# Optimization experiments

Measured on AMD Instinct MI355X. Metric: run time of the kernel, lower is better.

## Reference

```python
import jax, jax.numpy as jnp
import numpy as np
from jax import lax

B, A, SEQ, FIN = 512, 16, 50, 6
H, H2, T, G, S = 256, 128, 60, 64, 6
GR0, GR1 = -50.0, 50.0
CELL = (GR1 - GR0) / G
NTYPES, EMB = 10, 16
NENC, NL = 5, 2

def setup_inputs() -> dict:
    key = jax.random.key(0)
    ks = jax.random.split(key, 40)
    def rn(k, shape, scale=0.05):
        return (jax.random.normal(k, shape) * scale).astype(jnp.float32)
    history = jax.random.normal(ks[0], (B, A, SEQ, FIN), dtype=jnp.float32)
    types = jax.random.randint(ks[1], (B,), 0, NTYPES)
    history = history.at[:, 0, 0, 5].set(types.astype(jnp.float32))
    d = dict(history=history)
    d['emb'] = rn(ks[2], (NTYPES, EMB))
    d['fe_W1'] = rn(ks[3], (FIN + EMB, H)); d['fe_b1'] = jnp.zeros((H,), jnp.float32)
    d['fe_W2'] = rn(ks[4], (H, H));        d['fe_b2'] = jnp.zeros((H,), jnp.float32)
    d['enc_Wih'] = rn(ks[5], (NENC, NL, H, 3 * H))
    d['enc_Whh'] = rn(ks[6], (NENC, NL, H, 3 * H))
    d['enc_bih'] = rn(ks[7], (NENC, NL, 3 * H))
    d['enc_bhh'] = rn(ks[8], (NENC, NL, 3 * H))
    d['dec_Wih0'] = rn(ks[9], (2, 3 * H)); d['dec_Whh0'] = rn(ks[10], (H, 3 * H))
    d['dec_bih0'] = rn(ks[11], (3 * H));   d['dec_bhh0'] = rn(ks[12], (3 * H))
    d['dec_Wih1'] = rn(ks[13], (H, 3 * H)); d['dec_Whh1'] = rn(ks[14], (H, 3 * H))
    d['dec_bih1'] = rn(ks[15], (3 * H));    d['dec_bhh1'] = rn(ks[16], (3 * H))
    d['hg_W1'] = rn(ks[17], (H, H));   d['hg_b1'] = jnp.zeros((H,), jnp.float32)
    d['hg_W2'] = rn(ks[18], (H, H2));  d['hg_b2'] = jnp.zeros((H2,), jnp.float32)
    d['hg_W3'] = rn(ks[19], (H2, T * 2)); d['hg_b3'] = jnp.zeros((T * 2,), jnp.float32)
    d['ce_W1'] = rn(ks[20], (H, H2));  d['ce_b1'] = jnp.zeros((H2,), jnp.float32)
    d['ce_W2'] = rn(ks[21], (H2, T));  d['ce_b2'] = jnp.zeros((T,), jnp.float32)
    d['hp_W1'] = rn(ks[22], (H, H));   d['hp_b1'] = jnp.zeros((H,), jnp.float32)
    d['hp_W2'] = rn(ks[23], (H, G * G)); d['hp_b2'] = jnp.zeros((G * G,), jnp.float32)
    return d

def _gru_cell(xt, h, Wih, Whh, bih, bhh):
    # torch GRU gate order: r, z, n
    gi = xt @ Wih + bih
    gh = h @ Whh + bhh
    Hd = h.shape[-1]
    r = jax.nn.sigmoid(gi[:, :Hd] + gh[:, :Hd])
    z = jax.nn.sigmoid(gi[:, Hd:2 * Hd] + gh[:, Hd:2 * Hd])
    n = jnp.tanh(gi[:, 2 * Hd:] + r * gh[:, 2 * Hd:])
    return (1.0 - z) * n + z * h

def _forward(history, emb, fe_W1, fe_b1, fe_W2, fe_b2,
             enc_Wih, enc_Whh, enc_bih, enc_bhh,
             dec_Wih0, dec_Whh0, dec_bih0, dec_bhh0,
             dec_Wih1, dec_Whh1, dec_bih1, dec_bhh1,
             hg_W1, hg_b1, hg_W2, hg_b2, hg_W3, hg_b3,
             ce_W1, ce_b1, ce_W2, ce_b2, hp_W1, hp_b1, hp_W2, hp_b2):
    ego = history[:, 0]                                   # [B,SEQ,6]
    etype = jnp.clip(ego[:, 0, 5].astype(jnp.int32), 0, 9)
    # type -> encoder index (vehicle,pedestrian,cyclist,bus,default)
    eidx = jnp.array([0, 1, 4, 2, 3, 4, 4, 4, 4, 4], jnp.int32)[etype]
    te = emb[etype]                                       # [B,16]
    x_in = jnp.concatenate([ego, jnp.broadcast_to(te[:, None, :], (B, SEQ, EMB))], axis=-1)
    feat = jax.nn.relu(x_in @ fe_W1 + fe_b1) @ fe_W2 + fe_b2  # [B,SEQ,H]

    # 2-layer GRU with per-example (type-gathered) weights
    x_cur = feat.transpose(1, 0, 2)                       # [SEQ,B,H]
    h_finals = []
    for l in range(NL):
        Wih = enc_Wih[eidx, l]; Whh = enc_Whh[eidx, l]    # [B,H,3H]
        bih = enc_bih[eidx, l]; bhh = enc_bhh[eidx, l]    # [B,3H]
        def step(h, xt, Wih=Wih, Whh=Whh, bih=bih, bhh=bhh):
            gi = jnp.einsum('bd,bdg->bg', xt, Wih) + bih
            gh = jnp.einsum('bh,bhg->bg', h, Whh) + bhh
            r = jax.nn.sigmoid(gi[:, :H] + gh[:, :H])
            z = jax.nn.sigmoid(gi[:, H:2 * H] + gh[:, H:2 * H])
            n = jnp.tanh(gi[:, 2 * H:] + r * gh[:, 2 * H:])
            hn = (1.0 - z) * n + z * h
            return hn, hn
        h_last, ys = lax.scan(step, jnp.zeros((B, H), feat.dtype), x_cur)
        x_cur = ys
        h_finals.append(h_last)
    enc_h0, enc_h1 = h_finals

    # decoder GRU, single timestep: x = last ego position
    x0 = ego[:, -1, :2]
    h0 = _gru_cell(x0, enc_h0, dec_Wih0, dec_Whh0, dec_bih0, dec_bhh0)
    h1 = _gru_cell(h0, enc_h1, dec_Wih1, dec_Whh1, dec_bih1, dec_bhh1)
    last_hidden = h1                                      # [B,H]

    traj = (jax.nn.relu(jax.nn.relu(last_hidden @ hg_W1 + hg_b1) @ hg_W2 + hg_b2) @ hg_W3 + hg_b3)
    traj = traj.reshape(B, T, 2)
    conf = jax.nn.relu(last_hidden @ ce_W1 + ce_b1) @ ce_W2 + ce_b2   # [B,T]

    key = jax.random.key(42)
    k_noise, k_samp = jax.random.split(key)
    noise = jax.random.normal(k_noise, (T, B, H), last_hidden.dtype)
    scale = (0.1 * jnp.arange(T, dtype=last_hidden.dtype) / T)[:, None, None]
    th = last_hidden[None] + noise * scale                # [T,B,H]
    logits = jax.nn.relu(th @ hp_W1 + hp_b1) @ hp_W2 + hp_b2  # [T,B,G*G]

    # vectorized multinomial over (samples, timesteps, batch)
    idx = jax.random.categorical(k_samp, logits, shape=(S - 1, T, B))  # int [S-1,T,B]
    x_idx = (idx % G).astype(jnp.float32)
    y_idx = (idx // G).astype(jnp.float32)
    pts = jnp.stack([GR0 + x_idx * CELL + CELL / 2,
                     GR0 + y_idx * CELL + CELL / 2], axis=-1)  # [S-1,T,B,2]
    pts = pts.transpose(2, 0, 1, 3)                       # [B,S-1,T,2]

    predictions = jnp.concatenate([traj[:, None], pts], axis=1)  # [B,S,T,2]
    decay = jnp.float32(0.9) ** jnp.arange(S, dtype=jnp.float32)
    confidences = conf.mean(axis=1)[:, None] * decay[None, :]    # [B,S]
    return predictions, confidences

def reference(history, emb, fe_W1, fe_b1, fe_W2, fe_b2,
              enc_Wih, enc_Whh, enc_bih, enc_bhh,
              dec_Wih0, dec_Whh0, dec_bih0, dec_bhh0,
              dec_Wih1, dec_Whh1, dec_bih1, dec_bhh1,
              hg_W1, hg_b1, hg_W2, hg_b2, hg_W3, hg_b3,
              ce_W1, ce_b1, ce_W2, ce_b2, hp_W1, hp_b1, hp_W2, hp_b2):
    return _forward(history, emb, fe_W1, fe_b1, fe_W2, fe_b2,
                    enc_Wih, enc_Whh, enc_bih, enc_bhh,
                    dec_Wih0, dec_Whh0, dec_bih0, dec_bhh0,
                    dec_Wih1, dec_Whh1, dec_bih1, dec_bhh1,
                    hg_W1, hg_b1, hg_W2, hg_b2, hg_W3, hg_b3,
                    ce_W1, ce_b1, ce_W2, ce_b2, hp_W1, hp_b1, hp_W2, hp_b2)
```

## Files before the change

### kernel.cpp

```cpp
#include <hip/hip_runtime.h>
#include <stdint.h>
#include <math.h>

#define JAX_PARTITIONABLE 1

#define B_ 512
#define SEQ_ 50
#define H_ 256
#define H2_ 128
#define T_ 60
#define S_ 6
#define EMB_ 16
#define NL_ 2
#define TG_ 768
#define CAT_ 4096
#define GUMBEL_N 629145600u
#define NOISE_N 7864320u

typedef float f32x2 __attribute__((ext_vector_type(2)));

#define PKFMA_LO(acc, w, h) \
  asm("v_pk_fma_f32 %0, %1, %2, %0 op_sel:[0,0,0] op_sel_hi:[1,0,1]" : "+v"(acc) : "v"(w), "v"(h))
#define PKFMA_HI(acc, w, h) \
  asm("v_pk_fma_f32 %0, %1, %2, %0 op_sel:[0,1,0] op_sel_hi:[1,1,1]" : "+v"(acc) : "v"(w), "v"(h))

__host__ __device__ inline uint32_t rotl32(uint32_t x, int r) {
#if defined(__HIP_DEVICE_COMPILE__)
  return __builtin_amdgcn_alignbit(x, x, 32 - r);
#else
  return (x << r) | (x >> (32 - r));
#endif
}

__host__ __device__ inline void tf2x32(uint32_t k0, uint32_t k1, uint32_t x0, uint32_t x1,
                                       uint32_t& o0, uint32_t& o1) {
  uint32_t ks2 = k0 ^ k1 ^ 0x1BD11BDAu;
  x0 += k0; x1 += k1;
#define TFR(r) do { x0 += x1; x1 = rotl32(x1, r); x1 ^= x0; } while (0)
  TFR(13); TFR(15); TFR(26); TFR(6);
  x0 += k1; x1 += ks2 + 1u;
  TFR(17); TFR(29); TFR(16); TFR(24);
  x0 += ks2; x1 += k0 + 2u;
  TFR(13); TFR(15); TFR(26); TFR(6);
  x0 += k0; x1 += k1 + 3u;
  TFR(17); TFR(29); TFR(16); TFR(24);
  x0 += k1; x1 += ks2 + 4u;
  TFR(13); TFR(15); TFR(26); TFR(6);
  x0 += ks2; x1 += k0 + 5u;
#undef TFR
  o0 = x0; o1 = x1;
}

__device__ inline uint32_t jax_bits(uint32_t k0, uint32_t k1, uint32_t i, uint32_t n) {
#if JAX_PARTITIONABLE
  (void)n;
  uint32_t a, b;
  tf2x32(k0, k1, 0u, i, a, b);
  return a ^ b;
#else
  uint32_t half = n >> 1;
  uint32_t lo = (i < half) ? i : (i - half);
  uint32_t a, b;
  tf2x32(k0, k1, lo, lo + half, a, b);
  return (i < half) ? a : b;
#endif
}

__device__ inline float bits_to_f01(uint32_t bits) {
  return __uint_as_float((bits >> 9) | 0x3f800000u) - 1.0f;
}

__device__ inline float erfinv_f(float x) {
  double xd = (double)x;
  float w = (float)(-log((1.0 - xd) * (1.0 + xd)));
  float p;
  if (w < 5.0f) {
    w = __fadd_rn(w, -2.5f);
    p = 2.81022636e-08f;
    p = __fadd_rn(3.43273939e-07f, __fmul_rn(p, w));
    p = __fadd_rn(-3.5233877e-06f, __fmul_rn(p, w));
    p = __fadd_rn(-4.39150654e-06f, __fmul_rn(p, w));
    p = __fadd_rn(0.00021858087f, __fmul_rn(p, w));
    p = __fadd_rn(-0.00125372503f, __fmul_rn(p, w));
    p = __fadd_rn(-0.00417768164f, __fmul_rn(p, w));
    p = __fadd_rn(0.246640727f, __fmul_rn(p, w));
    p = __fadd_rn(1.50140941f, __fmul_rn(p, w));
  } else {
    w = __fadd_rn(__fsqrt_rn(w), -3.0f);
    p = -0.000200214257f;
    p = __fadd_rn(0.000100950558f, __fmul_rn(p, w));
    p = __fadd_rn(0.00134934322f, __fmul_rn(p, w));
    p = __fadd_rn(-0.00367342844f, __fmul_rn(p, w));
    p = __fadd_rn(0.00573950773f, __fmul_rn(p, w));
    p = __fadd_rn(-0.0076224613f, __fmul_rn(p, w));
    p = __fadd_rn(0.00943887047f, __fmul_rn(p, w));
    p = __fadd_rn(1.00167406f, __fmul_rn(p, w));
    p = __fadd_rn(2.83297682f, __fmul_rn(p, w));
  }
  return __fmul_rn(p, x);
}

__device__ inline float gumbel_f32(uint32_t bits) {
  float f = bits_to_f01(bits);
  float u = fmaxf(f, 1.17549435e-38f);
  float l1 = logf(u);
  return -logf(-l1);
}

__device__ inline uint32_t orderkey(float s) {
  uint32_t sb = __float_as_uint(s);
  return (sb & 0x80000000u) ? ~sb : (sb | 0x80000000u);
}

__global__ __launch_bounds__(512) void k_init(const float* __restrict__ hist,
                                              float* __restrict__ x0buf, int* __restrict__ ip) {
  int b = threadIdx.x;
  if (b < B_) {
    float tv = hist[b * 4800 + 5];
    int et = (int)tv;
    et = et < 0 ? 0 : (et > 9 ? 9 : et);
    const int mp[10] = {0, 1, 4, 2, 3, 4, 4, 4, 4, 4};
    ip[b] = et;
    ip[512 + b] = mp[et];
    x0buf[b * 2 + 0] = hist[b * 4800 + 49 * 6 + 0];
    x0buf[b * 2 + 1] = hist[b * 4800 + 49 * 6 + 1];
  }
  __syncthreads();
  if (b == 0) {
    int cnt[5] = {0, 0, 0, 0, 0};
    for (int i = 0; i < B_; i++) cnt[ip[512 + i]]++;
    int off[6];
    off[0] = 0;
    for (int e = 0; e < 5; e++) off[e + 1] = off[e] + cnt[e];
    int pos[5];
    for (int e = 0; e < 5; e++) pos[e] = off[e];
    for (int i = 0; i < B_; i++) { int e = ip[512 + i]; ip[1024 + pos[e]++] = i; }
    int* tbl = ip + 1536;
    int nrt = 0;
    for (int e = 0; e < 5; e++) {
      int n = cnt[e];
      for (int s = 0; s < n; s += 16) {
        tbl[1 + nrt] = e;
        tbl[37 + nrt] = off[e] + s;
        tbl[73 + nrt] = (n - s) < 16 ? (n - s) : 16;
        nrt++;
      }
    }
    tbl[0] = nrt;
  }
}

__global__ void k_zero(uint32_t* p, int n) {
  int i = blockIdx.x * blockDim.x + threadIdx.x;
  if (i < n) p[i] = 0u;
}

__global__ __launch_bounds__(256) void k_feat(const float* __restrict__ hist, const float* __restrict__ emb,
    const float* __restrict__ W1, const float* __restrict__ b1,
    const float* __restrict__ W2, const float* __restrict__ b2,
    const int* __restrict__ ip, float* __restrict__ featbuf) {
  __shared__ float xs[16][22];
  __shared__ float t1[16][H_];
  int row0 = blockIdx.x * 16;
  int tid = threadIdx.x;
  for (int idx = tid; idx < 16 * 22; idx += 256) {
    int r = idx / 22, c = idx % 22;
    int g = row0 + r;
    int b = g / SEQ_, s = g % SEQ_;
    xs[r][c] = (c < 6) ? hist[b * 4800 + s * 6 + c] : emb[ip[b] * EMB_ + (c - 6)];
  }
  __syncthreads();
  int j = tid;
  {
    double acc[16];
    for (int r = 0; r < 16; r++) acc[r] = 0.0;
    for (int k = 0; k < 22; k++) {
      double w = (double)W1[k * H_ + j];
      for (int r = 0; r < 16; r++) acc[r] += (double)xs[r][k] * w;
    }
    double bb = (double)b1[j];
    for (int r = 0; r < 16; r++) t1[r][j] = fmaxf((float)(acc[r] + bb), 0.0f);
  }
  __syncthreads();
  {
    double acc[16];
    for (int r = 0; r < 16; r++) acc[r] = 0.0;
    for (int k = 0; k < H_; k++) {
      double w = (double)W2[k * H_ + j];
      for (int r = 0; r < 16; r++) acc[r] += (double)t1[r][k] * w;
    }
    double bb = (double)b2[j];
    for (int r = 0; r < 16; r++) {
      float v = (float)(acc[r] + bb);
      int g = row0 + r;
      int b = g / SEQ_, s = g % SEQ_;
      featbuf[(size_t)s * (B_ * H_) + (size_t)b * H_ + j] = v;
    }
  }
}

__device__ __forceinline__ void gi_block(float (*xs)[H_], int* rowb,
    int rt, int cg, int tid,
    const float* __restrict__ x, float* __restrict__ gi_out,
    const float* __restrict__ Wih_base, const float* __restrict__ bih_base,
    int layer, const int* __restrict__ ip) {
  const int* tbl = ip + 1536;
  const int* order = ip + 1024;
  int nrt = tbl[0];
  if (rt >= nrt) return;
  int e = tbl[1 + rt];
  int start = tbl[37 + rt];
  int nr = tbl[73 + rt];
  for (int idx = tid; idx < 16 * H_; idx += 256) {
    int r = idx >> 8, k = idx & 255;
    int rr = (r < nr) ? r : 0;
    int b = order[start + rr];
    if (k == 0) rowb[r] = b;
    xs[r][k] = x[b * H_ + k];
  }
  __syncthreads();
  size_t woff = (size_t)(e * NL_ + layer);
  const float* Wih = Wih_base + woff * (size_t)H_ * TG_;
  const float* bih = bih_base + woff * TG_;
  int j = tid & 31, rs = tid >> 5;
  int c = cg * 32 + j;
  int cr = c, cz = H_ + c, cn = 2 * H_ + c;
  double ar0 = 0, ar1 = 0, az0 = 0, az1 = 0, an0 = 0, an1 = 0;
  for (int k = 0; k < H_; k++) {
    float wr = Wih[k * TG_ + cr], wz = Wih[k * TG_ + cz], wn = Wih[k * TG_ + cn];
    float x0 = xs[rs][k], x1 = xs[rs + 8][k];
    ar0 += (double)x0 * wr; ar1 += (double)x1 * wr;
    az0 += (double)x0 * wz; az1 += (double)x1 * wz;
    an0 += (double)x0 * wn; an1 += (double)x1 * wn;
  }
  double br = (double)bih[cr], bz = (double)bih[cz], bn = (double)bih[cn];
  for (int p = 0; p < 2; p++) {
    int r = rs + 8 * p;
    if (r >= nr) continue;
    int b = rowb[r];
    gi_out[b * TG_ + cr] = (float)((p ? ar1 : ar0) + br);
    gi_out[b * TG_ + cz] = (float)((p ? az1 : az0) + bz);
    gi_out[b * TG_ + cn] = (float)((p ? an1 : an0) + bn);
  }
}

__device__ __forceinline__ void step_block(float (*hs)[H_], int* rowb,
    int rt, int cg, int tid,
    const float* __restrict__ gi_in, const float* __restrict__ hin,
    float* __restrict__ hout, float* __restrict__ ys,
    const float* __restrict__ Whh_base, const float* __restrict__ bhh_base,
    int layer, const int* __restrict__ ip) {
  const int* tbl = ip + 1536;
  const int* order = ip + 1024;
  int nrt = tbl[0];
  if (rt >= nrt) return;
  int e = tbl[1 + rt];
  int start = tbl[37 + rt];
  int nr = tbl[73 + rt];
  for (int idx = tid; idx < 16 * H_; idx += 256) {
    int r = idx >> 8, k = idx & 255;
    int rr = (r < nr) ? r : 0;
    int b = order[start + rr];
    if (k == 0) rowb[r] = b;
    hs[r][k] = hin[b * H_ + k];
  }
  __syncthreads();
  size_t woff = (size_t)(e * NL_ + layer);
  const float* Whh = Whh_base + woff * (size_t)H_ * TG_;
  const float* bhh = bhh_base + woff * TG_;
  int j = tid & 31, rs = tid >> 5;
  int c = cg * 32 + j;
  int cr = c, cz = H_ + c, cn = 2 * H_ + c;
  double gr0 = 0, gr1 = 0, gz0 = 0, gz1 = 0, gn0 = 0, gn1 = 0;
  for (int k = 0; k < H_; k++) {
    float wr = Whh[k * TG_ + cr], wz = Whh[k * TG_ + cz], wn = Whh[k * TG_ + cn];
    float h0 = hs[rs][k], h1 = hs[rs + 8][k];
    gr0 += (double)h0 * wr; gr1 += (double)h1 * wr;
    gz0 += (double)h0 * wz; gz1 += (double)h1 * wz;
    gn0 += (double)h0 * wn; gn1 += (double)h1 * wn;
  }
  double bhr = (double)bhh[cr], bhz = (double)bhh[cz], bhn = (double)bhh[cn];
  for (int p = 0; p < 2; p++) {
    int r = rs + 8 * p;
    if (r >= nr) continue;
    int b = rowb[r];
    double gir = (double)gi_in[b * TG_ + cr];
    double giz = (double)gi_in[b * TG_ + cz];
    double gin = (double)gi_in[b * TG_ + cn];
    double ghr = (p ? gr1 : gr0) + bhr;
    double ghz = (p ? gz1 : gz0) + bhz;
    double ghn = (p ? gn1 : gn0) + bhn;
    double rr = 1.0 / (1.0 + exp(-(gir + ghr)));
    double zz = 1.0 / (1.0 + exp(-(giz + ghz)));
    double nn = tanh(gin + rr * ghn);
    double hv = (double)hs[r][c];
    float hnew = (float)((1.0 - zz) * nn + zz * hv);
    hout[b * H_ + c] = hnew;
    if (ys) ys[b * H_ + c] = hnew;
  }
}

__global__ __launch_bounds__(256) void k_pipe(int d,
    const float* __restrict__ feat, float* __restrict__ ys0,
    float* __restrict__ gi0, float* __restrict__ gi1,
    float* __restrict__ h0A, float* __restrict__ h0B,
    float* __restrict__ h1A, float* __restrict__ h1B,
    const float* __restrict__ Wih, const float* __restrict__ Whh,
    const float* __restrict__ bih, const float* __restrict__ bhh,
    const int* __restrict__ ip) {
  __shared__ float sb[16][H_];
  __shared__ int rowb[16];
  int g = blockIdx.x;
  int grp = g / 288, bx = g % 288;
  int rt = bx >> 3, cg = bx & 7;
  int tid = threadIdx.x;
  if (grp == 0) {
    int t = d; if (t >= SEQ_) return;
    gi_block(sb, rowb, rt, cg, tid, feat + (size_t)t * 131072,
             gi0 + (size_t)(t & 1) * 393216, Wih, bih, 0, ip);
  } else if (grp == 1) {
    int t = d - 1; if (t < 0 || t >= SEQ_) return;
    const float* hin = (t & 1) ? h0B : h0A;
    float* hout = (t & 1) ? h0A : h0B;
    step_block(sb, rowb, rt, cg, tid, gi0 + (size_t)(t & 1) * 393216,
               hin, hout, ys0 + (size_t)t * 131072, Whh, bhh, 0, ip);
  } else if (grp == 2) {
    int t = d - 2; if (t < 0 || t >= SEQ_) return;
    gi_block(sb, rowb, rt, cg, tid, ys0 + (size_t)t * 131072,
             gi1 + (size_t)(t & 1) * 393216, Wih, bih, 1, ip);
  } else {
    int t = d - 3; if (t < 0 || t >= SEQ_) return;
    const float* hin = (t & 1) ? h1B : h1A;
    float* hout = (t & 1) ? h1A : h1B;
    step_block(sb, rowb, rt, cg, tid, gi1 + (size_t)(t & 1) * 393216,
               hin, hout, nullptr, Whh, bhh, 1, ip);
  }
}

template <int D1>
__global__ __launch_bounds__(256) void k_gru(
    const float* __restrict__ x, const float* __restrict__ hin,
    float* __restrict__ hout,
    const float* __restrict__ Wih, const float* __restrict__ Whh,
    const float* __restrict__ bih, const float* __restrict__ bhh) {
  __shared__ float xs[16][(D1 == 2) ? 2 : H_];
  __shared__ float hs[16][H_];
  int bx = blockIdx.x, by = blockIdx.y;
  int start = bx * 16;
  int tid = threadIdx.x;
  for (int idx = tid; idx < 16 * H_; idx += 256) {
    int r = idx >> 8, k = idx & 255;
    int b = start + r;
    hs[r][k] = hin[b * H_ + k];
    if (D1 == H_) xs[r][k] = x[b * H_ + k];
    else if (k < D1) xs[r][k] = x[b * D1 + k];
  }
  __syncthreads();
  int j = tid & 31, rs = tid >> 5;
  int hc = by * 32 + j;
  int cr = hc, cz = H_ + hc, cn = 2 * H_ + hc;
  double ra0 = 0, ra1 = 0, za0 = 0, za1 = 0, ni0 = 0, ni1 = 0, nh0 = 0, nh1 = 0;
  for (int k = 0; k < H_; k++) {
    float wrh = Whh[k * TG_ + cr], wzh = Whh[k * TG_ + cz], wnh = Whh[k * TG_ + cn];
    float h0v = hs[rs][k], h1v = hs[rs + 8][k];
    ra0 += (double)h0v * wrh; ra1 += (double)h1v * wrh;
    za0 += (double)h0v * wzh; za1 += (double)h1v * wzh;
    nh0 += (double)h0v * wnh; nh1 += (double)h1v * wnh;
    if (D1 == H_) {
      float wri = Wih[k * TG_ + cr], wzi = Wih[k * TG_ + cz], wni = Wih[k * TG_ + cn];
      float x0v = xs[rs][k], x1v = xs[rs + 8][k];
      ra0 += (double)x0v * wri; ra1 += (double)x1v * wri;
      za0 += (double)x0v * wzi; za1 += (double)x1v * wzi;
      ni0 += (double)x0v * wni; ni1 += (double)x1v * wni;
    }
  }
  if (D1 != H_) {
    for (int k = 0; k < D1; k++) {
      float wri = Wih[k * TG_ + cr], wzi = Wih[k * TG_ + cz], wni = Wih[k * TG_ + cn];
      float x0v = xs[rs][k], x1v = xs[rs + 8][k];
      ra0 += (double)x0v * wri; ra1 += (double)x1v * wri;
      za0 += (double)x0v * wzi; za1 += (double)x1v * wzi;
      ni0 += (double)x0v * wni; ni1 += (double)x1v * wni;
    }
  }
  double br_i = (double)bih[cr], bz_i = (double)bih[cz], bn_i = (double)bih[cn];
  double br_h = (double)bhh[cr], bz_h = (double)bhh[cz], bn_h = (double)bhh[cn];
  for (int p = 0; p < 2; p++) {
    int r = rs + 8 * p;
    double ra = p ? ra1 : ra0, za = p ? za1 : za0, ni = p ? ni1 : ni0, nh = p ? nh1 : nh0;
    double rr = 1.0 / (1.0 + exp(-(ra + br_i + br_h)));
    double zz = 1.0 / (1.0 + exp(-(za + bz_i + bz_h)));
    double nn = tanh((ni + bn_i) + rr * (nh + bn_h));
    double hv = (double)hs[r][hc];
    float hnew = (float)((1.0 - zz) * nn + zz * hv);
    hout[(start + r) * H_ + hc] = hnew;
  }
}

__global__ __launch_bounds__(256) void k_heads(const float* __restrict__ lh,
    const float* __restrict__ hgW1, const float* __restrict__ hgb1,
    const float* __restrict__ hgW2, const float* __restrict__ hgb2,
    const float* __restrict__ hgW3, const float* __restrict__ hgb3,
    const float* __restrict__ ceW1, const float* __restrict__ ceb1,
    const float* __restrict__ ceW2, const float* __restrict__ ceb2,
    float* __restrict__ out) {
  __shared__ float hsm[16][H_];
  __shared__ float t1[16][H_];
  __shared__ float t2[16][H2_];
  __shared__ float c2s[16][T_];
  int row0 = blockIdx.x * 16;
  int tid = threadIdx.x;
  for (int idx = tid; idx < 16 * H_; idx += 256) {
    int r = idx >> 8, k = idx & 255;
    hsm[r][k] = lh[(size_t)(row0 + r) * H_ + k];
  }
  __syncthreads();
  {
    int j = tid;
    for (int r = 0; r < 16; r++) {
      double a = 0;
      for (int k = 0; k < H_; k++) a += (double)hsm[r][k] * (double)hgW1[k * H_ + j];
      t1[r][j] = fmaxf((float)(a + (double)hgb1[j]), 0.0f);
    }
  }
  __syncthreads();
  if (tid < H2_) {
    int j = tid;
    for (int r = 0; r < 16; r++) {
      double a = 0;
      for (int k = 0; k < H_; k++) a += (double)t1[r][k] * (double)hgW2[k * H2_ + j];
      t2[r][j] = fmaxf((float)(a + (double)hgb2[j]), 0.0f);
    }
  }
  __syncthreads();
  if (tid < 2 * T_) {
    int j = tid;
    for (int r = 0; r < 16; r++) {
      double a = 0;
      for (int k = 0; k < H2_; k++) a += (double)t2[r][k] * (double)hgW3[k * (2 * T_) + j];
      float v = (float)(a + (double)hgb3[j]);
      int b = row0 + r;
      int t = j >> 1, c = j & 1;
      out[(((size_t)b * S_ + 0) * T_ + t) * 2 + c] = v;
    }
  }
  __syncthreads();
  if (tid < H2_) {
    int j = tid;
    for (int r = 0; r < 16; r++) {
      double a = 0;
      for (int k = 0; k < H_; k++) a += (double)hsm[r][k] * (double)ceW1[k * H2_ + j];
      t2[r][j] = fmaxf((float)(a + (double)ceb1[j]), 0.0f);
    }
  }
  __syncthreads();
  if (tid < T_) {
    int j = tid;
    for (int r = 0; r < 16; r++) {
      double a = 0;
      for (int k = 0; k < H2_; k++) a += (double)t2[r][k] * (double)ceW2[k * T_ + j];
      c2s[r][j] = (float)(a + (double)ceb2[j]);
    }
  }
  __syncthreads();
  if (tid < 16) {
    int r = tid;
    int b = row0 + r;
    double s = 0;
    for (int j = 0; j < T_; j++) s += (double)c2s[r][j];
    float m = (float)(s / 60.0);
    for (int sd = 0; sd < S_; sd++) {
      float d = (float)pow((double)0.9f, (double)sd);
      out[368640 + b * S_ + sd] = __fmul_rn(m, d);
    }
  }
}

__global__ __launch_bounds__(256) void k_hp1(const float* __restrict__ lh,
    const float* __restrict__ W1, const float* __restrict__ b1,
    float* __restrict__ h1buf, uint32_t nk0, uint32_t nk1) {
  __shared__ float th[16][H_];
  int row0 = blockIdx.x * 16;
  int tid = threadIdx.x;
  const float SQRT2F = 1.4142135623730951f;
  const float LO = -0x1.fffffep-1f;
  for (int idx = tid; idx < 16 * H_; idx += 256) {
    int r = idx >> 8, k = idx & 255;
    int g = row0 + r;
    int t = g / B_, b = g % B_;
    uint32_t i = ((uint32_t)t * B_ + (uint32_t)b) * H_ + (uint32_t)k;
    uint32_t bits = jax_bits(nk0, nk1, i, NOISE_N);
    float f = bits_to_f01(bits);
    float u = fmaxf(LO, __fadd_rn(__fmul_rn(f, 2.0f), LO));
    float nz = __fmul_rn(SQRT2F, erfinv_f(u));
    float sc = __fdiv_rn(__fmul_rn(0.1f, (float)t), 60.0f);
    th[r][k] = __fadd_rn(lh[(size_t)b * H_ + k], __fmul_rn(nz, sc));
  }
  __syncthreads();
  int j = tid;
  double acc[16];
  for (int r = 0; r < 16; r++) acc[r] = 0.0;
  for (int k = 0; k < H_; k++) {
    double w = (double)W1[k * H_ + j];
    for (int r = 0; r < 16; r++) acc[r] += (double)th[r][k] * w;
  }
  double bb = (double)b1[j];
  for (int r = 0; r < 16; r++)
    h1buf[(size_t)(row0 + r) * H_ + j] = fmaxf((float)(acc[r] + bb), 0.0f);
}

__global__ __launch_bounds__(256) void k_hp2(const float* __restrict__ h1buf,
    const float* __restrict__ W2, const float* __restrict__ b2,
    unsigned long long* __restrict__ samples, uint32_t sk0, uint32_t sk1) {
  __shared__ float h1[16][H_];
  int row0 = blockIdx.x * 16;
  int cat0 = blockIdx.y * 256;
  int tid = threadIdx.x;
  for (int idx = tid; idx < 16 * H_ / 4; idx += 256) {
    int r = idx >> 6, k4 = (idx & 63) << 2;
    *(float4*)&h1[r][k4] = *(const float4*)&h1buf[(size_t)(row0 + r) * H_ + k4];
  }
  __syncthreads();
  int wave = tid >> 6;
  int lane = tid & 63;
  int catA = cat0 + 4 * lane;
  int rbase = 4 * wave;

  f32x2 acc[4][2];
#pragma unroll
  for (int r = 0; r < 4; r++) { acc[r][0] = (f32x2)0.0f; acc[r][1] = (f32x2)0.0f; }
  const float* w2p = W2 + catA;
  for (int k = 0; k < H_; k += 4) {
    float4 hv[4];
    hv[0] = *(const float4*)&h1[rbase + 0][k];
    hv[1] = *(const float4*)&h1[rbase + 1][k];
    hv[2] = *(const float4*)&h1[rbase + 2][k];
    hv[3] = *(const float4*)&h1[rbase + 3][k];
    float4 wv[4];
#pragma unroll
    for (int kk = 0; kk < 4; kk++) wv[kk] = *(const float4*)&w2p[(size_t)(k + kk) * CAT_];
#pragma unroll
    for (int kk = 0; kk < 4; kk++) {
      f32x2 wlo; wlo.x = wv[kk].x; wlo.y = wv[kk].y;
      f32x2 whi; whi.x = wv[kk].z; whi.y = wv[kk].w;
#pragma unroll
      for (int r = 0; r < 4; r++) {
        f32x2 hp;
        if (kk & 2) { hp.x = (&hv[r].x)[2]; hp.y = (&hv[r].x)[3]; }
        else        { hp.x = (&hv[r].x)[0]; hp.y = (&hv[r].x)[1]; }
        if (kk & 1) { PKFMA_HI(acc[r][0], wlo, hp); PKFMA_HI(acc[r][1], whi, hp); }
        else        { PKFMA_LO(acc[r][0], wlo, hp); PKFMA_LO(acc[r][1], whi, hp); }
      }
    }
  }
  float lg[4][4];
  float4 b4 = *(const float4*)&b2[catA];
#pragma unroll
  for (int r = 0; r < 4; r++) {
    lg[r][0] = __fadd_rn(acc[r][0].x, b4.x);
    lg[r][1] = __fadd_rn(acc[r][0].y, b4.y);
    lg[r][2] = __fadd_rn(acc[r][1].x, b4.z);
    lg[r][3] = __fadd_rn(acc[r][1].y, b4.w);
  }

  int t = row0 / B_;
  int bbase = row0 % B_;
#pragma unroll
  for (int s = 0; s < S_ - 1; s++) {
#pragma unroll
    for (int q = 0; q < 4; q++) {
      int brow = bbase + rbase + q;
      uint32_t ibase = (((uint32_t)s * T_ + (uint32_t)t) * B_ + (uint32_t)brow) * CAT_ + (uint32_t)catA;
      float sc0 = __fadd_rn(gumbel_f32(jax_bits(sk0, sk1, ibase + 0u, GUMBEL_N)), lg[q][0]);
      float sc1 = __fadd_rn(gumbel_f32(jax_bits(sk0, sk1, ibase + 1u, GUMBEL_N)), lg[q][1]);
      float sc2 = __fadd_rn(gumbel_f32(jax_bits(sk0, sk1, ibase + 2u, GUMBEL_N)), lg[q][2]);
      float sc3 = __fadd_rn(gumbel_f32(jax_bits(sk0, sk1, ibase + 3u, GUMBEL_N)), lg[q][3]);
      float bs = sc0; int bc = catA;
      if (sc1 > bs) { bs = sc1; bc = catA + 1; }
      if (sc2 > bs) { bs = sc2; bc = catA + 2; }
      if (sc3 > bs) { bs = sc3; bc = catA + 3; }
      float mv = bs;
      for (int off = 1; off < 64; off <<= 1)
        mv = fmaxf(mv, __shfl_xor(mv, off, 64));
      unsigned long long mask = __ballot(bs == mv);
      int src = __ffsll(mask) - 1;
      int wcat = __shfl(bc, src, 64);
      if (lane == 0) {
        unsigned long long p =
            (((unsigned long long)orderkey(mv)) << 32) | (unsigned long long)(~(uint32_t)wcat);
        atomicMax(&samples[((size_t)s * T_ + t) * B_ + brow], p);
      }
    }
  }
}

__global__ void k_emit(const unsigned long long* __restrict__ samples, float* __restrict__ out) {
  int gid = blockIdx.x * blockDim.x + threadIdx.x;
  if (gid >= (S_ - 1) * T_ * B_) return;
  int b = gid % B_;
  int t = (gid / B_) % T_;
  int s = gid / (B_ * T_);
  unsigned long long v = samples[gid];
  uint32_t cat = ~(uint32_t)(v & 0xFFFFFFFFu);
  float xi = (float)(cat & 63u);
  float yi = (float)(cat >> 6);
  float px = -50.0f + xi * 1.5625f + 0.78125f;
  float py = -50.0f + yi * 1.5625f + 0.78125f;
  size_t o = (((size_t)b * S_ + (size_t)(s + 1)) * T_ + t) * 2;
  out[o] = px;
  out[o + 1] = py;
}

extern "C" void kernel_launch(void* const* d_in, const int* in_sizes, int n_in,
                              void* d_out, int out_size, void* d_ws, size_t ws_size,
                              hipStream_t stream) {
  (void)in_sizes; (void)n_in; (void)out_size; (void)ws_size;
  const float* hist   = (const float*)d_in[0];
  const float* emb    = (const float*)d_in[1];
  const float* feW1   = (const float*)d_in[2];
  const float* feb1   = (const float*)d_in[3];
  const float* feW2   = (const float*)d_in[4];
  const float* feb2   = (const float*)d_in[5];
  const float* encWih = (const float*)d_in[6];
  const float* encWhh = (const float*)d_in[7];
  const float* encbih = (const float*)d_in[8];
  const float* encbhh = (const float*)d_in[9];
  const float* dWih0  = (const float*)d_in[10];
  const float* dWhh0  = (const float*)d_in[11];
  const float* dbih0  = (const float*)d_in[12];
  const float* dbhh0  = (const float*)d_in[13];
  const float* dWih1  = (const float*)d_in[14];
  const float* dWhh1  = (const float*)d_in[15];
  const float* dbih1  = (const float*)d_in[16];
  const float* dbhh1  = (const float*)d_in[17];
  const float* hgW1   = (const float*)d_in[18];
  const float* hgb1   = (const float*)d_in[19];
  const float* hgW2   = (const float*)d_in[20];
  const float* hgb2   = (const float*)d_in[21];
  const float* hgW3   = (const float*)d_in[22];
  const float* hgb3   = (const float*)d_in[23];
  const float* ceW1   = (const float*)d_in[24];
  const float* ceb1   = (const float*)d_in[25];
  const float* ceW2   = (const float*)d_in[26];
  const float* ceb2   = (const float*)d_in[27];
  const float* hpW1   = (const float*)d_in[28];
  const float* hpb1   = (const float*)d_in[29];
  const float* hpW2   = (const float*)d_in[30];
  const float* hpb2   = (const float*)d_in[31];
  float* out = (float*)d_out;
  float* ws = (float*)d_ws;

  float* feat  = ws;
  float* ys0   = ws + 6553600;
  float* gi0   = ws + 13107200;
  float* gi1   = ws + 13893632;
  float* h0A   = ws + 14680064;
  float* h0B   = h0A + 131072;
  float* h1A   = h0B + 131072;
  float* h1B   = h1A + 131072;
  float* dech0 = h1B + 131072;
  float* lh    = dech0 + 131072;
  float* x0buf = lh + 131072;
  int*   ip    = (int*)(x0buf + 1024);
  unsigned long long* samples =
      (unsigned long long*)(((uintptr_t)(ip + 2048) + 255) & ~(uintptr_t)255);
  float* h1hp  = ws;

  uint32_t kn0, kn1, ks0, ks1;
#if JAX_PARTITIONABLE
  tf2x32(0u, 42u, 0u, 0u, kn0, kn1);
  tf2x32(0u, 42u, 0u, 1u, ks0, ks1);
#else
  { uint32_t a0, a1, b0, b1;
    tf2x32(0u, 42u, 0u, 2u, a0, a1);
    tf2x32(0u, 42u, 1u, 3u, b0, b1);
    kn0 = a0; kn1 = b0; ks0 = a1; ks1 = b1; }
#endif

  k_init<<<dim3(1), dim3(512), 0, stream>>>(hist, x0buf, ip);
  k_zero<<<dim3((524288 + 255) / 256), dim3(256), 0, stream>>>((uint32_t*)h0A, 524288);
  k_zero<<<dim3((307200 + 255) / 256), dim3(256), 0, stream>>>((uint32_t*)samples, 307200);
  k_feat<<<dim3(1600), dim3(256), 0, stream>>>(hist, emb, feW1, feb1, feW2, feb2, ip, feat);

  for (int d = 0; d < SEQ_ + 3; d++) {
    k_pipe<<<dim3(1152), dim3(256), 0, stream>>>(d,
        feat, ys0, gi0, gi1, h0A, h0B, h1A, h1B,
        encWih, encWhh, encbih, encbhh, ip);
  }

  k_gru<2><<<dim3(32, 8), dim3(256), 0, stream>>>(
      x0buf, h0A, dech0, dWih0, dWhh0, dbih0, dbhh0);
  k_gru<H_><<<dim3(32, 8), dim3(256), 0, stream>>>(
      dech0, h1A, lh, dWih1, dWhh1, dbih1, dbhh1);

  k_heads<<<dim3(32), dim3(256), 0, stream>>>(lh, hgW1, hgb1, hgW2, hgb2, hgW3, hgb3,
                                              ceW1, ceb1, ceW2, ceb2, out);
  k_hp1<<<dim3(1920), dim3(256), 0, stream>>>(lh, hpW1, hpb1, h1hp, kn0, kn1);
  k_hp2<<<dim3(1920, 16), dim3(256), 0, stream>>>(h1hp, hpW2, hpb2, samples, ks0, ks1);
  k_emit<<<dim3(600), dim3(256), 0, stream>>>(samples, out);
}
```

Before: 5.837 ms.

## Prepack encoder GRU weights into per-column float4 gate triples

```diff
diff --git a/kernel.cpp b/kernel.cpp
--- a/kernel.cpp
+++ b/kernel.cpp
@@ -155,6 +155,25 @@
   if (i < n) p[i] = 0u;
 }
 
+__global__ __launch_bounds__(256) void k_pack(const float* __restrict__ Wih,
+                                              const float* __restrict__ Whh,
+                                              float4* __restrict__ wp) {
+  int i = blockIdx.x * 256 + threadIdx.x;
+  if (i >= 20 * 65536) return;
+  int k = i & 255;
+  int c = (i >> 8) & 255;
+  int em = i >> 16;
+  int m = em & 1;
+  int el = em >> 1;
+  const float* W = (m ? Whh : Wih) + (size_t)el * H_ * TG_;
+  float4 v;
+  v.x = W[k * TG_ + c];
+  v.y = W[k * TG_ + H_ + c];
+  v.z = W[k * TG_ + 2 * H_ + c];
+  v.w = 0.0f;
+  wp[((size_t)em * 256 + c) * 256 + k] = v;
+}
+
 __global__ __launch_bounds__(256) void k_feat(const float* __restrict__ hist, const float* __restrict__ emb,
     const float* __restrict__ W1, const float* __restrict__ b1,
     const float* __restrict__ W2, const float* __restrict__ b2,
@@ -199,7 +218,128 @@
   }
 }
 
-__device__ __forceinline__ void gi_block(float (*xs)[H_], int* rowb,
+__device__ __forceinline__ void gi_block_p(float (*xs)[H_], int* rowb,
+    int rt, int cg, int tid,
+    const float* __restrict__ x, float* __restrict__ gi_out,
+    const float4* __restrict__ wpack, const float* __restrict__ bih_base,
+    int layer, const int* __restrict__ ip) {
+  const int* tbl = ip + 1536;
+  const int* order = ip + 1024;
+  int nrt = tbl[0];
+  if (rt >= nrt) return;
+  int e = tbl[1 + rt];
+  int start = tbl[37 + rt];
+  int nr = tbl[73 + rt];
+  for (int idx = tid; idx < 16 * H_; idx += 256) {
+    int r = idx >> 8, k = idx & 255;
+    int rr = (r < nr) ? r : 0;
+    int b = order[start + rr];
+    if (k == 0) rowb[r] = b;
+    xs[r][k] = x[b * H_ + k];
+  }
+  __syncthreads();
+  int j = tid & 31, rs = tid >> 5;
+  int c = cg * 32 + j;
+  int el = e * NL_ + layer;
+  const float4* wp = wpack + ((size_t)(el * 2 + 0) * 256 + c) * 256;
+  const float* bih = bih_base + (size_t)el * TG_;
+  double ar0 = 0, ar1 = 0, az0 = 0, az1 = 0, an0 = 0, an1 = 0;
+  for (int k = 0; k < H_; k += 4) {
+    float4 w0 = wp[k], w1 = wp[k + 1], w2 = wp[k + 2], w3 = wp[k + 3];
+    float4 xa = *(const float4*)&xs[rs][k];
+    float4 xb = *(const float4*)&xs[rs + 8][k];
+    ar0 += (double)xa.x * (double)w0.x; ar1 += (double)xb.x * (double)w0.x;
+    az0 += (double)xa.x * (double)w0.y; az1 += (double)xb.x * (double)w0.y;
+    an0 += (double)xa.x * (double)w0.z; an1 += (double)xb.x * (double)w0.z;
+    ar0 += (double)xa.y * (double)w1.x; ar1 += (double)xb.y * (double)w1.x;
+    az0 += (double)xa.y * (double)w1.y; az1 += (double)xb.y * (double)w1.y;
+    an0 += (double)xa.y * (double)w1.z; an1 += (double)xb.y * (double)w1.z;
+    ar0 += (double)xa.z * (double)w2.x; ar1 += (double)xb.z * (double)w2.x;
+    az0 += (double)xa.z * (double)w2.y; az1 += (double)xb.z * (double)w2.y;
+    an0 += (double)xa.z * (double)w2.z; an1 += (double)xb.z * (double)w2.z;
+    ar0 += (double)xa.w * (double)w3.x; ar1 += (double)xb.w * (double)w3.x;
+    az0 += (double)xa.w * (double)w3.y; az1 += (double)xb.w * (double)w3.y;
+    an0 += (double)xa.w * (double)w3.z; an1 += (double)xb.w * (double)w3.z;
+  }
+  int cr = c, cz = H_ + c, cn = 2 * H_ + c;
+  double br = (double)bih[cr], bz = (double)bih[cz], bn = (double)bih[cn];
+  for (int p = 0; p < 2; p++) {
+    int r = rs + 8 * p;
+    if (r >= nr) continue;
+    int b = rowb[r];
+    gi_out[b * TG_ + cr] = (float)((p ? ar1 : ar0) + br);
+    gi_out[b * TG_ + cz] = (float)((p ? az1 : az0) + bz);
+    gi_out[b * TG_ + cn] = (float)((p ? an1 : an0) + bn);
+  }
+}
+
+__device__ __forceinline__ void step_block_p(float (*hs)[H_], int* rowb,
+    int rt, int cg, int tid,
+    const float* __restrict__ gi_in, const float* __restrict__ hin,
+    float* __restrict__ hout, float* __restrict__ ys,
+    const float4* __restrict__ wpack, const float* __restrict__ bhh_base,
+    int layer, const int* __restrict__ ip) {
+  const int* tbl = ip + 1536;
+  const int* order = ip + 1024;
+  int nrt = tbl[0];
+  if (rt >= nrt) return;
+  int e = tbl[1 + rt];
+  int start = tbl[37 + rt];
+  int nr = tbl[73 + rt];
+  for (int idx = tid; idx < 16 * H_; idx += 256) {
+    int r = idx >> 8, k = idx & 255;
+    int rr = (r < nr) ? r : 0;
+    int b = order[start + rr];
+    if (k == 0) rowb[r] = b;
+    hs[r][k] = hin[b * H_ + k];
+  }
+  __syncthreads();
+  int j = tid & 31, rs = tid >> 5;
+  int c = cg * 32 + j;
+  int el = e * NL_ + layer;
+  const float4* wp = wpack + ((size_t)(el * 2 + 1) * 256 + c) * 256;
+  const float* bhh = bhh_base + (size_t)el * TG_;
+  double gr0 = 0, gr1 = 0, gz0 = 0, gz1 = 0, gn0 = 0, gn1 = 0;
+  for (int k = 0; k < H_; k += 4) {
+    float4 w0 = wp[k], w1 = wp[k + 1], w2 = wp[k + 2], w3 = wp[k + 3];
+    float4 ha = *(const float4*)&hs[rs][k];
+    float4 hb = *(const float4*)&hs[rs + 8][k];
+    gr0 += (double)ha.x * (double)w0.x; gr1 += (double)hb.x * (double)w0.x;
+    gz0 += (double)ha.x * (double)w0.y; gz1 += (double)hb.x * (double)w0.y;
+    gn0 += (double)ha.x * (double)w0.z; gn1 += (double)hb.x * (double)w0.z;
+    gr0 += (double)ha.y * (double)w1.x; gr1 += (double)hb.y * (double)w1.x;
+    gz0 += (double)ha.y * (double)w1.y; gz1 += (double)hb.y * (double)w1.y;
+    gn0 += (double)ha.y * (double)w1.z; gn1 += (double)hb.y * (double)w1.z;
+    gr0 += (double)ha.z * (double)w2.x; gr1 += (double)hb.z * (double)w2.x;
+    gz0 += (double)ha.z * (double)w2.y; gz1 += (double)hb.z * (double)w2.y;
+    gn0 += (double)ha.z * (double)w2.z; gn1 += (double)hb.z * (double)w2.z;
+    gr0 += (double)ha.w * (double)w3.x; gr1 += (double)hb.w * (double)w3.x;
+    gz0 += (double)ha.w * (double)w3.y; gz1 += (double)hb.w * (double)w3.y;
+    gn0 += (double)ha.w * (double)w3.z; gn1 += (double)hb.w * (double)w3.z;
+  }
+  int cr = c, cz = H_ + c, cn = 2 * H_ + c;
+  double bhr = (double)bhh[cr], bhz = (double)bhh[cz], bhn = (double)bhh[cn];
+  for (int p = 0; p < 2; p++) {
+    int r = rs + 8 * p;
+    if (r >= nr) continue;
+    int b = rowb[r];
+    double gir = (double)gi_in[b * TG_ + cr];
+    double giz = (double)gi_in[b * TG_ + cz];
+    double gin = (double)gi_in[b * TG_ + cn];
+    double ghr = (p ? gr1 : gr0) + bhr;
+    double ghz = (p ? gz1 : gz0) + bhz;
+    double ghn = (p ? gn1 : gn0) + bhn;
+    double rr = 1.0 / (1.0 + exp(-(gir + ghr)));
+    double zz = 1.0 / (1.0 + exp(-(giz + ghz)));
+    double nn = tanh(gin + rr * ghn);
+    double hv = (double)hs[r][c];
+    float hnew = (float)((1.0 - zz) * nn + zz * hv);
+    hout[b * H_ + c] = hnew;
+    if (ys) ys[b * H_ + c] = hnew;
+  }
+}
+
+__device__ __forceinline__ void gi_block_u(float (*xs)[H_], int* rowb,
     int rt, int cg, int tid,
     const float* __restrict__ x, float* __restrict__ gi_out,
     const float* __restrict__ Wih_base, const float* __restrict__ bih_base,
@@ -244,7 +384,7 @@
   }
 }
 
-__device__ __forceinline__ void step_block(float (*hs)[H_], int* rowb,
+__device__ __forceinline__ void step_block_u(float (*hs)[H_], int* rowb,
     int rt, int cg, int tid,
     const float* __restrict__ gi_in, const float* __restrict__ hin,
     float* __restrict__ hout, float* __restrict__ ys,
@@ -300,6 +440,7 @@
   }
 }
 
+template <bool PACKED>
 __global__ __launch_bounds__(256) void k_pipe(int d,
     const float* __restrict__ feat, float* __restrict__ ys0,
     float* __restrict__ gi0, float* __restrict__ gi1,
@@ -307,7 +448,7 @@
     float* __restrict__ h1A, float* __restrict__ h1B,
     const float* __restrict__ Wih, const float* __restrict__ Whh,
     const float* __restrict__ bih, const float* __restrict__ bhh,
-    const int* __restrict__ ip) {
+    const float4* __restrict__ wpack, const int* __restrict__ ip) {
   __shared__ float sb[16][H_];
   __shared__ int rowb[16];
   int g = blockIdx.x;
@@ -316,24 +457,32 @@
   int tid = threadIdx.x;
   if (grp == 0) {
     int t = d; if (t >= SEQ_) return;
-    gi_block(sb, rowb, rt, cg, tid, feat + (size_t)t * 131072,
-             gi0 + (size_t)(t & 1) * 393216, Wih, bih, 0, ip);
+    if (PACKED) gi_block_p(sb, rowb, rt, cg, tid, feat + (size_t)t * 131072,
+                           gi0 + (size_t)(t & 1) * 393216, wpack, bih, 0, ip);
+    else        gi_block_u(sb, rowb, rt, cg, tid, feat + (size_t)t * 131072,
+                           gi0 + (size_t)(t & 1) * 393216, Wih, bih, 0, ip);
   } else if (grp == 1) {
     int t = d - 1; if (t < 0 || t >= SEQ_) return;
     const float* hin = (t & 1) ? h0B : h0A;
     float* hout = (t & 1) ? h0A : h0B;
-    step_block(sb, rowb, rt, cg, tid, gi0 + (size_t)(t & 1) * 393216,
-               hin, hout, ys0 + (size_t)t * 131072, Whh, bhh, 0, ip);
+    if (PACKED) step_block_p(sb, rowb, rt, cg, tid, gi0 + (size_t)(t & 1) * 393216,
+                             hin, hout, ys0 + (size_t)t * 131072, wpack, bhh, 0, ip);
+    else        step_block_u(sb, rowb, rt, cg, tid, gi0 + (size_t)(t & 1) * 393216,
+                             hin, hout, ys0 + (size_t)t * 131072, Whh, bhh, 0, ip);
   } else if (grp == 2) {
     int t = d - 2; if (t < 0 || t >= SEQ_) return;
-    gi_block(sb, rowb, rt, cg, tid, ys0 + (size_t)t * 131072,
-             gi1 + (size_t)(t & 1) * 393216, Wih, bih, 1, ip);
+    if (PACKED) gi_block_p(sb, rowb, rt, cg, tid, ys0 + (size_t)t * 131072,
+                           gi1 + (size_t)(t & 1) * 393216, wpack, bih, 1, ip);
+    else        gi_block_u(sb, rowb, rt, cg, tid, ys0 + (size_t)t * 131072,
+                           gi1 + (size_t)(t & 1) * 393216, Wih, bih, 1, ip);
   } else {
     int t = d - 3; if (t < 0 || t >= SEQ_) return;
     const float* hin = (t & 1) ? h1B : h1A;
     float* hout = (t & 1) ? h1A : h1B;
-    step_block(sb, rowb, rt, cg, tid, gi1 + (size_t)(t & 1) * 393216,
-               hin, hout, nullptr, Whh, bhh, 1, ip);
+    if (PACKED) step_block_p(sb, rowb, rt, cg, tid, gi1 + (size_t)(t & 1) * 393216,
+                             hin, hout, nullptr, wpack, bhh, 1, ip);
+    else        step_block_u(sb, rowb, rt, cg, tid, gi1 + (size_t)(t & 1) * 393216,
+                             hin, hout, nullptr, Whh, bhh, 1, ip);
   }
 }
 
@@ -614,7 +763,7 @@
 extern "C" void kernel_launch(void* const* d_in, const int* in_sizes, int n_in,
                               void* d_out, int out_size, void* d_ws, size_t ws_size,
                               hipStream_t stream) {
-  (void)in_sizes; (void)n_in; (void)out_size; (void)ws_size;
+  (void)in_sizes; (void)n_in; (void)out_size;
   const float* hist   = (const float*)d_in[0];
   const float* emb    = (const float*)d_in[1];
   const float* feW1   = (const float*)d_in[2];
@@ -666,6 +815,11 @@
       (unsigned long long*)(((uintptr_t)(ip + 2048) + 255) & ~(uintptr_t)255);
   float* h1hp  = ws;
 
+  size_t samples_end = (size_t)((char*)(samples + 307200) - (char*)ws);
+  size_t wpack_off = (samples_end + 255) & ~(size_t)255;
+  float4* wpack = (float4*)((char*)ws + wpack_off);
+  bool packed = (wpack_off + (size_t)20 * 65536 * 16) <= ws_size;
+
   uint32_t kn0, kn1, ks0, ks1;
 #if JAX_PARTITIONABLE
   tf2x32(0u, 42u, 0u, 0u, kn0, kn1);
@@ -680,12 +834,19 @@
   k_init<<<dim3(1), dim3(512), 0, stream>>>(hist, x0buf, ip);
   k_zero<<<dim3((524288 + 255) / 256), dim3(256), 0, stream>>>((uint32_t*)h0A, 524288);
   k_zero<<<dim3((307200 + 255) / 256), dim3(256), 0, stream>>>((uint32_t*)samples, 307200);
+  if (packed)
+    k_pack<<<dim3(5120), dim3(256), 0, stream>>>(encWih, encWhh, wpack);
   k_feat<<<dim3(1600), dim3(256), 0, stream>>>(hist, emb, feW1, feb1, feW2, feb2, ip, feat);
 
   for (int d = 0; d < SEQ_ + 3; d++) {
-    k_pipe<<<dim3(1152), dim3(256), 0, stream>>>(d,
-        feat, ys0, gi0, gi1, h0A, h0B, h1A, h1B,
-        encWih, encWhh, encbih, encbhh, ip);
+    if (packed)
+      k_pipe<true><<<dim3(1152), dim3(256), 0, stream>>>(d,
+          feat, ys0, gi0, gi1, h0A, h0B, h1A, h1B,
+          encWih, encWhh, encbih, encbhh, wpack, ip);
+    else
+      k_pipe<false><<<dim3(1152), dim3(256), 0, stream>>>(d,
+          feat, ys0, gi0, gi1, h0A, h0B, h1A, h1B,
+          encWih, encWhh, encbih, encbhh, wpack, ip);
   }
 
   k_gru<2><<<dim3(32, 8), dim3(256), 0, stream>>>(
```

Measured after the change: 11.02 ms. +88.9%, slower.
